# Kernel tuning notes

Hardware: AMD Instinct MI355X
Metric: run time of the kernel (lower is better)

## Reference

```python
import jax, jax.numpy as jnp
import numpy as np

B, N, E = 64, 512, 8192          # graphs, nodes per graph, edges per graph
F_IN, H, C = 128, 128, 10        # in features, hidden, classes
K1, K2 = 256, 128                # dense pool cluster counts: ceil(.5*N), ceil(.5*K1)
EPS = 1e-15


def setup_inputs():
    key = jax.random.key(0)
    keys = jax.random.split(key, 32)
    it = iter(keys)
    def w(shape, fan_in):
        return jax.random.normal(next(it), shape, jnp.float32) / np.sqrt(fan_in)
    x = jax.random.normal(next(it), (B * N, F_IN), jnp.float32)
    src_l = jax.random.randint(next(it), (B, E), 0, N)
    dst_l = jax.random.randint(next(it), (B, E), 0, N)
    off = (jnp.arange(B) * N)[:, None]
    src = (src_l + off).reshape(-1).astype(jnp.int32)
    dst = (dst_l + off).reshape(-1).astype(jnp.int32)
    return dict(
        x=x, src=src, dst=dst,
        conv0_wr=w((F_IN, H), F_IN), conv0_wroot=w((F_IN, H), F_IN), conv0_b=jnp.zeros((H,), jnp.float32),
        sconv2_wr=w((H, H), H), sconv2_wroot=w((H, H), H), sconv2_b=jnp.zeros((H,), jnp.float32),
        sconv3_wr=w((H, H), H), sconv3_wroot=w((H, H), H), sconv3_b=jnp.zeros((H,), jnp.float32),
        sage1_wr=w((H, H), H), sage1_wroot=w((H, H), H), sage1_b=jnp.zeros((H,), jnp.float32),
        sage2_wr=w((H, H), H), sage2_wroot=w((H, H), H), sage2_b=jnp.zeros((H,), jnp.float32),
        pool0_w=w((H, K1), H), pool0_b=jnp.zeros((K1,), jnp.float32),
        pool1_w=w((H, K2), H), pool1_b=jnp.zeros((K2,), jnp.float32),
        p1=w((H,), H), p2=w((H,), H), p3=w((H,), H),
        lin1_1_w=w((2 * H, H), 2 * H), lin1_1_b=jnp.zeros((H,), jnp.float32),
        lin1_w=w((H, H), H), lin1_b=jnp.zeros((H,), jnp.float32),
        lin2_w=w((2 * H, C), 2 * H), lin2_b=jnp.zeros((C,), jnp.float32),
    )


def _graph_conv(x, src, dst, emask, wr, wroot, b, n):
    # PyG GraphConv: lin_rel(sum_j x_j) + lin_root(x_i); invalid edges masked to 0.
    msg = x[src] * emask[:, None]
    agg = jax.ops.segment_sum(msg, dst, num_segments=n)
    return agg @ wr + x @ wroot + b


def _topk_pool(x, score_w, src, dst, emask, n_per_graph, k):
    # TopK pooling (MPoolS): score = x.w/||w||, keep top ratio*n per graph, gate by tanh(score).
    score = x @ score_w / (jnp.linalg.norm(score_w) + 1e-16)
    idx = jax.lax.top_k(score.reshape(B, n_per_graph), k)[1]
    perm = (idx + (jnp.arange(B) * n_per_graph)[:, None]).reshape(-1)
    new_x = x[perm] * jnp.tanh(score[perm])[:, None]
    new_id = jnp.full((B * n_per_graph,), -1, jnp.int32).at[perm].set(
        jnp.arange(B * k, dtype=jnp.int32))
    ns, nd = new_id[src], new_id[dst]
    valid = (ns >= 0) & (nd >= 0) & (emask > 0)
    return new_x, jnp.where(valid, ns, 0), jnp.where(valid, nd, 0), valid.astype(x.dtype)


def _readout(x, k):
    # gmp || gap per graph (nodes are contiguous, k per graph)
    xr = x.reshape(B, k, -1)
    return jnp.concatenate([xr.max(axis=1), xr.mean(axis=1)], axis=-1)


def _dense_sage(x, adj, wr, wroot, b):
    agg = (adj @ x) / jnp.clip(adj.sum(-1, keepdims=True), 1.0, None)
    return agg @ wr + x @ wroot + b


def _dense_mincut_pool(x, adj, s):
    s = jax.nn.softmax(s, axis=-1)
    k = s.shape[-1]
    out = jnp.einsum('bnk,bnf->bkf', s, x)
    out_adj = jnp.einsum('bnk,bnm,bml->bkl', s, adj, s)
    mincut_num = jnp.trace(out_adj, axis1=-2, axis2=-1)
    deg = adj.sum(-1)
    mincut_den = jnp.einsum('bn,bnk,bnk->b', deg, s, s)
    mc = -jnp.mean(mincut_num / (mincut_den + EPS))
    ss = jnp.einsum('bnk,bnl->bkl', s, s)
    ss_n = jnp.linalg.norm(ss, axis=(1, 2), keepdims=True)
    eye = jnp.eye(k, dtype=x.dtype)
    o = jnp.mean(jnp.linalg.norm(ss / (ss_n + EPS) - eye / jnp.sqrt(k), axis=(1, 2)))
    di = jnp.arange(k)
    out_adj = out_adj.at[:, di, di].set(0.0)
    dpool = jnp.sqrt(out_adj.sum(-1)) + EPS
    out_adj = out_adj / dpool[:, :, None] / dpool[:, None, :]
    return out, out_adj, mc, o


def _forward(x, src, dst, conv0_wr, conv0_wroot, conv0_b, sconv2_wr, sconv2_wroot, sconv2_b,
             sconv3_wr, sconv3_wroot, sconv3_b, sage1_wr, sage1_wroot, sage1_b,
             sage2_wr, sage2_wroot, sage2_b, pool0_w, pool0_b, pool1_w, pool1_b,
             p1, p2, p3, lin1_1_w, lin1_1_b, lin1_w, lin1_b, lin2_w, lin2_b):
    relu = jax.nn.relu
    e0 = jnp.ones((src.shape[0],), x.dtype)
    x0 = relu(_graph_conv(x, src, dst, e0, conv0_wr, conv0_wroot, conv0_b, B * N))
    # ---- sparse (MPoolS / top-k) branch, stage 1 ----
    sx, s1, d1, m1 = _topk_pool(x0, p1, src, dst, e0, N, N // 2)
    sx1 = _readout(sx, N // 2)
    # ---- dense (DiffPool-style) branch ----
    xd = x0.reshape(B, N, H)                               # to_dense_batch (full mask)
    g = src // N
    adj = jnp.zeros((B, N, N), x.dtype).at[g, src % N, dst % N].add(1.0)  # to_dense_adj
    s = xd @ pool0_w + pool0_b
    xd, adj, mc, o = _dense_mincut_pool(xd, adj, s)
    xd = relu(_dense_sage(xd, adj, sage1_wr, sage1_wroot, sage1_b))
    s = xd @ pool1_w + pool1_b
    xd, adj, mc2, o2 = _dense_mincut_pool(xd, adj, s)
    mc, o = mc + mc2, o + o2
    xd = _dense_sage(xd, adj, sage2_wr, sage2_wroot, sage2_b)
    xg = relu(xd.mean(axis=1) @ lin1_w + lin1_b)
    # ---- sparse branch, stages 2 and 3 ----
    sx = relu(_graph_conv(sx, s1, d1, m1, sconv2_wr, sconv2_wroot, sconv2_b, B * (N // 2)))
    sx, s2, d2, m2 = _topk_pool(sx, p2, s1, d1, m1, N // 2, N // 4)
    sx2 = _readout(sx, N // 4)
    sx = relu(_graph_conv(sx, s2, d2, m2, sconv3_wr, sconv3_wroot, sconv3_b, B * (N // 4)))
    sx, s3, d3, m3 = _topk_pool(sx, p3, s2, d2, m2, N // 4, N // 8)
    sx3 = _readout(sx, N // 8)
    sxr = relu((sx1 + sx2 + sx3) @ lin1_1_w + lin1_1_b)
    logits = jnp.concatenate([sxr, xg], axis=-1) @ lin2_w + lin2_b
    return logits, mc, o


def reference(x, src, dst, conv0_wr, conv0_wroot, conv0_b, sconv2_wr, sconv2_wroot, sconv2_b,
              sconv3_wr, sconv3_wroot, sconv3_b, sage1_wr, sage1_wroot, sage1_b,
              sage2_wr, sage2_wroot, sage2_b, pool0_w, pool0_b, pool1_w, pool1_b,
              p1, p2, p3, lin1_1_w, lin1_1_b, lin1_w, lin1_b, lin2_w, lin2_b):
    return _forward(x, src, dst, conv0_wr, conv0_wroot, conv0_b, sconv2_wr, sconv2_wroot,
                    sconv2_b, sconv3_wr, sconv3_wroot, sconv3_b, sage1_wr, sage1_wroot,
                    sage1_b, sage2_wr, sage2_wroot, sage2_b, pool0_w, pool0_b, pool1_w,
                    pool1_b, p1, p2, p3, lin1_1_w, lin1_1_b, lin1_w, lin1_b, lin2_w, lin2_b)
```

## Files before the change

### kernel.cpp

```cpp
#include <hip/hip_runtime.h>
#include <math.h>

#define NGRAPH 64
#define NE 524288
#define EPG 8192
#define TSZ 2560

typedef short s16x8 __attribute__((ext_vector_type(8)));
typedef float f32x4 __attribute__((ext_vector_type(4)));

__device__ inline unsigned short f2bf(float f) {
    unsigned int u = __float_as_uint(f);
    return (unsigned short)((u + 0x7FFFu + ((u >> 16) & 1u)) >> 16);
}
__device__ inline float bf2f(unsigned short h) {
    return __uint_as_float((unsigned int)h << 16);
}
__device__ inline unsigned int f2pk(float v) {
    unsigned short h = f2bf(v);
    return (unsigned int)h | ((unsigned int)f2bf(v - bf2f(h)) << 16);
}

__global__ void edge_count2(const int* __restrict__ keyA, int* __restrict__ cntA,
                            const int* __restrict__ keyB, int* __restrict__ cntB) {
    int e = blockIdx.x * 256 + threadIdx.x;
    if (e >= NE) return;
    if (blockIdx.y == 0) atomicAdd(&cntA[keyA[e]], 1);
    else                 atomicAdd(&cntB[keyB[e]], 1);
}

__device__ inline void scan_body(const int* __restrict__ counts, int* __restrict__ offs,
                                 int* __restrict__ cursor, int nPerGraph,
                                 float* __restrict__ degOut, int* s) {
    const int g = blockIdx.x, t = threadIdx.x;
    int v = (t < nPerGraph) ? counts[g * nPerGraph + t] : 0;
    s[t] = v; __syncthreads();
    for (int d = 1; d < 512; d <<= 1) {
        int u = (t >= d) ? s[t - d] : 0;
        __syncthreads();
        s[t] += u;
        __syncthreads();
    }
    if (t < nPerGraph) {
        int o = g * EPG + s[t] - v;
        offs[g * nPerGraph + t] = o;
        cursor[g * nPerGraph + t] = o;
        if (degOut) degOut[g * nPerGraph + t] = (float)v;
    }
}

__global__ __launch_bounds__(512) void scan_offsets(const int* __restrict__ counts,
        int* __restrict__ offs, int* __restrict__ cursor, int nPerGraph,
        float* __restrict__ degOut) {
    __shared__ int s[512];
    scan_body(counts, offs, cursor, nPerGraph, degOut, s);
}

__global__ __launch_bounds__(512) void scan_offsets2(
        const int* __restrict__ cA, int* __restrict__ oA, int* __restrict__ uA,
        const int* __restrict__ cB, int* __restrict__ oB, int* __restrict__ uB,
        int nPerGraph, float* __restrict__ degB) {
    __shared__ int s[512];
    if (blockIdx.y == 0) scan_body(cA, oA, uA, nPerGraph, nullptr, s);
    else                 scan_body(cB, oB, uB, nPerGraph, degB, s);
}

__global__ void edge_fill(const int* __restrict__ key, const int* __restrict__ payload,
                          const float* __restrict__ mask, int* __restrict__ cursor,
                          int* __restrict__ elist) {
    int e = blockIdx.x * 256 + threadIdx.x;
    if (e < NE && (!mask || mask[e] > 0.f)) {
        int p = atomicAdd(&cursor[key[e]], 1);
        elist[p] = payload[e];
    }
}

__global__ void edge_fill2(const int* __restrict__ kA, const int* __restrict__ pA,
                           int* __restrict__ uA, int* __restrict__ eA,
                           const int* __restrict__ kB, const int* __restrict__ pB,
                           int* __restrict__ uB, int* __restrict__ eB) {
    int e = blockIdx.x * 256 + threadIdx.x;
    if (e >= NE) return;
    if (blockIdx.y == 0) { int p = atomicAdd(&uA[kA[e]], 1); eA[p] = pA[e]; }
    else                 { int p = atomicAdd(&uB[kB[e]], 1); eB[p] = pB[e]; }
}

__device__ inline void addpk(float4& acc, uint4 u) {
    acc.x += __uint_as_float(u.x << 16) + __uint_as_float(u.x & 0xffff0000u);
    acc.y += __uint_as_float(u.y << 16) + __uint_as_float(u.y & 0xffff0000u);
    acc.z += __uint_as_float(u.z << 16) + __uint_as_float(u.z & 0xffff0000u);
    acc.w += __uint_as_float(u.w << 16) + __uint_as_float(u.w & 0xffff0000u);
}

__global__ __launch_bounds__(256) void gather_csr(
    const float* __restrict__ xf, const unsigned int* __restrict__ xp, int Fx,
    const int* __restrict__ offs, const int* __restrict__ cnts,
    const int* __restrict__ elist,
    unsigned int* __restrict__ opk,
    int totRows, int rowsPerGraph)
{
    const int gid = (blockIdx.x * 256 + threadIdx.x) >> 5;
    const int lane = threadIdx.x & 31;
    const int csh = (Fx == 256) ? 1 : 0;
    const int rid = gid >> csh;
    const int c0 = (gid & ((1 << csh) - 1)) << 7;
    if (rid >= totRows) return;
    const int row = (rid & 63) * rowsPerGraph + (rid >> 6);
    const int beg = offs[row];
    const int n = cnts[row];
    const long long co = (long long)c0 + (lane << 2);
    float4 acc = make_float4(0.f, 0.f, 0.f, 0.f);
    int j = 0;
    if (xp) {
        for (; j + 4 <= n; j += 4) {
            const int n0 = elist[beg + j], n1 = elist[beg + j + 1];
            const int n2 = elist[beg + j + 2], n3 = elist[beg + j + 3];
            const uint4 u0 = *(const uint4*)&xp[(long long)n0 * Fx + co];
            const uint4 u1 = *(const uint4*)&xp[(long long)n1 * Fx + co];
            const uint4 u2 = *(const uint4*)&xp[(long long)n2 * Fx + co];
            const uint4 u3 = *(const uint4*)&xp[(long long)n3 * Fx + co];
            addpk(acc, u0); addpk(acc, u1); addpk(acc, u2); addpk(acc, u3);
        }
        for (; j < n; ++j)
            addpk(acc, *(const uint4*)&xp[(long long)elist[beg + j] * Fx + co]);
    } else {
        for (; j + 4 <= n; j += 4) {
            const int n0 = elist[beg + j], n1 = elist[beg + j + 1];
            const int n2 = elist[beg + j + 2], n3 = elist[beg + j + 3];
            const float4 v0 = *(const float4*)&xf[(long long)n0 * Fx + co];
            const float4 v1 = *(const float4*)&xf[(long long)n1 * Fx + co];
            const float4 v2 = *(const float4*)&xf[(long long)n2 * Fx + co];
            const float4 v3 = *(const float4*)&xf[(long long)n3 * Fx + co];
            acc.x += v0.x + v1.x + v2.x + v3.x;
            acc.y += v0.y + v1.y + v2.y + v3.y;
            acc.z += v0.z + v1.z + v2.z + v3.z;
            acc.w += v0.w + v1.w + v2.w + v3.w;
        }
        for (; j < n; ++j) {
            const float4 v = *(const float4*)&xf[(long long)elist[beg + j] * Fx + co];
            acc.x += v.x; acc.y += v.y; acc.z += v.z; acc.w += v.w;
        }
    }
    uint4 pk;
    pk.x = f2pk(acc.x); pk.y = f2pk(acc.y); pk.z = f2pk(acc.z); pk.w = f2pk(acc.w);
    *(uint4*)&opk[(long long)row * Fx + co] = pk;
}

struct WSpec {
    const float* w1; const float* w2; int K1; int K2; int Nn;
    unsigned short* oh; unsigned short* ol;
};

__global__ void wconv_all(WSpec s0, WSpec s1, WSpec s2, WSpec s3, WSpec s4, WSpec s5, WSpec s6) {
    WSpec s;
    switch (blockIdx.y) {
        case 0: s = s0; break; case 1: s = s1; break; case 2: s = s2; break;
        case 3: s = s3; break; case 4: s = s4; break; case 5: s = s5; break;
        default: s = s6; break;
    }
    int idx = blockIdx.x * 256 + threadIdx.x;
    int Kt = s.K1 + s.K2;
    if (idx >= s.Nn * Kt) return;
    int n = idx / Kt, k = idx - n * Kt;
    float v = (k < s.K1) ? s.w1[(long long)k * s.Nn + n] : s.w2[(long long)(k - s.K1) * s.Nn + n];
    unsigned short h = f2bf(v);
    s.oh[idx] = h;
    s.ol[idx] = f2bf(v - __uint_as_float((unsigned int)h << 16));
}

__device__ inline void stageN_split(const float* __restrict__ src, int ldk, int k0,
                                    short* lds, int tid) {
    const int r = tid >> 2, kq = (tid & 3) << 3;
    const float* p = src + (long long)r * ldk + k0 + kq;
    float v[8];
    *(float4*)v = *(const float4*)p;
    *(float4*)(v + 4) = *(const float4*)(p + 4);
    s16x8 hv, lv;
    #pragma unroll
    for (int i = 0; i < 8; ++i) {
        unsigned short h = f2bf(v[i]);
        float hf = __uint_as_float((unsigned int)h << 16);
        hv[i] = (short)h;
        lv[i] = (short)f2bf(v[i] - hf);
    }
    *(s16x8*)(lds + r * 40 + kq) = hv;
    *(s16x8*)(lds + TSZ + r * 40 + kq) = lv;
}

__device__ inline void stageN_pk(const unsigned int* __restrict__ src, int ldk, int k0,
                                 short* lds, int tid) {
    const int r = tid >> 2, kq = (tid & 3) << 3;
    const unsigned int* p = src + (long long)r * ldk + k0 + kq;
    uint4 a = *(const uint4*)p;
    uint4 b = *(const uint4*)(p + 4);
    uint4 hw, lw;
    hw.x = (a.x & 0xffffu) | (a.y << 16);
    hw.y = (a.z & 0xffffu) | (a.w << 16);
    hw.z = (b.x & 0xffffu) | (b.y << 16);
    hw.w = (b.z & 0xffffu) | (b.w << 16);
    lw.x = (a.x >> 16) | (a.y & 0xffff0000u);
    lw.y = (a.z >> 16) | (a.w & 0xffff0000u);
    lw.z = (b.x >> 16) | (b.y & 0xffff0000u);
    lw.w = (b.z >> 16) | (b.w & 0xffff0000u);
    *(uint4*)(lds + r * 40 + kq) = hw;
    *(uint4*)(lds + TSZ + r * 40 + kq) = lw;
}

__device__ inline void stageT_pk(const unsigned int* __restrict__ P,
                                 int ldm, int k0, int m0, short* lds, int tid) {
    const int kp = tid >> 4, mc = tid & 15;
    const int k = kp << 1;
    const unsigned int* p0 = P + (long long)(k0 + k) * ldm + m0 + mc;
    const unsigned int* p1 = p0 + ldm;
    #pragma unroll
    for (int i = 0; i < 4; ++i) {
        unsigned int e0 = p0[i << 4], e1 = p1[i << 4];
        const int o = (mc + (i << 4)) * 40 + k;
        *(unsigned int*)(lds + o) = (e0 & 0xffffu) | (e1 << 16);
        *(unsigned int*)(lds + o + TSZ) = (e0 >> 16) | (e1 & 0xffff0000u);
    }
}

__device__ inline void stageW_split(const unsigned short* __restrict__ wh,
                                    const unsigned short* __restrict__ wl, int ldk,
                                    int n0, int k0, short* lds, int tid) {
    const int r = tid >> 2, kq = (tid & 3) << 3;
    *(s16x8*)(lds + r * 40 + kq) = *(const s16x8*)(wh + (long long)(n0 + r) * ldk + k0 + kq);
    *(s16x8*)(lds + TSZ + r * 40 + kq) = *(const s16x8*)(wl + (long long)(n0 + r) * ldk + k0 + kq);
}

__device__ inline void loadT8(const unsigned int* __restrict__ P, int ldm, int k0, int m0,
                              int tid, unsigned int (&r)[8]) {
    const int kp = tid >> 4, mc = tid & 15;
    const int k = kp << 1;
    const unsigned int* p0 = P + (long long)(k0 + k) * ldm + m0 + mc;
    const unsigned int* p1 = p0 + ldm;
    #pragma unroll
    for (int i = 0; i < 4; ++i) { r[i] = p0[i << 4]; r[4 + i] = p1[i << 4]; }
}
__device__ inline void storeT8(short* lds, int tid, const unsigned int (&r)[8]) {
    const int kp = tid >> 4, mc = tid & 15;
    const int k = kp << 1;
    #pragma unroll
    for (int i = 0; i < 4; ++i) {
        unsigned int e0 = r[i], e1 = r[4 + i];
        const int o = (mc + (i << 4)) * 40 + k;
        *(unsigned int*)(lds + o) = (e0 & 0xffffu) | (e1 << 16);
        *(unsigned int*)(lds + o + TSZ) = (e0 >> 16) | (e1 & 0xffff0000u);
    }
}
__device__ inline void storeT8_hi(short* lds, int tid, const unsigned int (&r)[8]) {
    const int kp = tid >> 4, mc = tid & 15;
    const int k = kp << 1;
    #pragma unroll
    for (int i = 0; i < 4; ++i)
        *(unsigned int*)(lds + (mc + (i << 4)) * 40 + k) =
            (r[i] & 0xffffu) | (r[4 + i] << 16);
}

__device__ inline void mfma_split(const short* As, const short* Bs, int wm, int wn,
                                  int l15, int quad, f32x4 (&acc)[2][2]) {
    const int ko = quad << 3;
    s16x8 ah[2], al[2], bh[2], bl[2];
    #pragma unroll
    for (int i = 0; i < 2; ++i) {
        const int ra = (wm + (i << 4) + l15) * 40 + ko;
        const int rb = (wn + (i << 4) + l15) * 40 + ko;
        ah[i] = *(const s16x8*)&As[ra];
        al[i] = *(const s16x8*)&As[TSZ + ra];
        bh[i] = *(const s16x8*)&Bs[rb];
        bl[i] = *(const s16x8*)&Bs[TSZ + rb];
    }
    #pragma unroll
    for (int mi = 0; mi < 2; ++mi)
    #pragma unroll
    for (int ni = 0; ni < 2; ++ni) {
        f32x4 c = acc[mi][ni];
        c = __builtin_amdgcn_mfma_f32_16x16x32_bf16(ah[mi], bh[ni], c, 0, 0, 0);
        c = __builtin_amdgcn_mfma_f32_16x16x32_bf16(ah[mi], bl[ni], c, 0, 0, 0);
        c = __builtin_amdgcn_mfma_f32_16x16x32_bf16(al[mi], bh[ni], c, 0, 0, 0);
        acc[mi][ni] = c;
    }
}

__device__ inline void mfma_hi(const short* As, const short* Bs, int wm, int wn,
                               int l15, int quad, f32x4 (&acc)[2][2]) {
    const int ko = quad << 3;
    s16x8 ah[2], bh[2];
    #pragma unroll
    for (int i = 0; i < 2; ++i) {
        ah[i] = *(const s16x8*)&As[(wm + (i << 4) + l15) * 40 + ko];
        bh[i] = *(const s16x8*)&Bs[(wn + (i << 4) + l15) * 40 + ko];
    }
    #pragma unroll
    for (int mi = 0; mi < 2; ++mi)
    #pragma unroll
    for (int ni = 0; ni < 2; ++ni)
        acc[mi][ni] = __builtin_amdgcn_mfma_f32_16x16x32_bf16(ah[mi], bh[ni], acc[mi][ni], 0, 0, 0);
}

__global__ __launch_bounds__(256) void gemm_aw(
    const unsigned int* __restrict__ A1p, const float* __restrict__ A1f, int K1,
    const unsigned int* __restrict__ A2p, const float* __restrict__ A2f, int K2,
    const unsigned short* __restrict__ Wh, const unsigned short* __restrict__ Wl,
    const float* __restrict__ bias, float* __restrict__ C,
    unsigned int* __restrict__ Cpk,
    int Nn, int doRelu)
{
    __shared__ short As[2 * TSZ], Bs[2 * TSZ];
    const int m0 = blockIdx.y << 6, n0 = blockIdx.x << 6;
    const int tid = threadIdx.x, lane = tid & 63, wv = tid >> 6;
    const int l15 = lane & 15, quad = lane >> 4;
    const int wm = (wv & 1) << 5, wn = (wv >> 1) << 5;
    f32x4 acc[2][2] = {};
    const int Kt = K1 + K2;
    for (int k0 = 0; k0 < Kt; k0 += 32) {
        if (k0 < K1) {
            if (A1p) stageN_pk(A1p + (long long)m0 * K1, K1, k0, As, tid);
            else     stageN_split(A1f + (long long)m0 * K1, K1, k0, As, tid);
        } else {
            if (A2p) stageN_pk(A2p + (long long)m0 * K2, K2, k0 - K1, As, tid);
            else     stageN_split(A2f + (long long)m0 * K2, K2, k0 - K1, As, tid);
        }
        stageW_split(Wh, Wl, Kt, n0, k0, Bs, tid);
        __syncthreads();
        mfma_split(As, Bs, wm, wn, l15, quad, acc);
        __syncthreads();
    }
    #pragma unroll
    for (int mi = 0; mi < 2; ++mi)
    #pragma unroll
    for (int ni = 0; ni < 2; ++ni) {
        const int col = n0 + wn + (ni << 4) + l15;
        const float bv = bias ? bias[col] : 0.f;
        #pragma unroll
        for (int r = 0; r < 4; ++r) {
            const int row = m0 + wm + (mi << 4) + (quad << 2) + r;
            float v = acc[mi][ni][r] + bv;
            if (doRelu) v = fmaxf(v, 0.f);
            if (C)   C[(long long)row * Nn + col] = v;
            if (Cpk) Cpk[(long long)row * Nn + col] = f2pk(v);
        }
    }
}

struct TTSet {
    const unsigned int* Bp;
    float* C; unsigned int* Cpk; float* fro;
    int Nn; int dual;
    long long sB, sC;
};

__global__ __launch_bounds__(256) void gemm_tt(
    const unsigned int* __restrict__ Ap, int Kd, int Mm, long long sA,
    int zsplit, TTSet t0, TTSet t1)
{
    __shared__ short As[2 * TSZ], Bs[2 * TSZ], A2s[TSZ];
    __shared__ float redf[4];
    const int z = blockIdx.x;
    int nz = blockIdx.z;
    const TTSet tt = (nz < zsplit) ? t0 : t1;
    if (blockIdx.z >= zsplit) nz -= zsplit;
    const unsigned int* Apz = Ap + (long long)z * sA;
    const unsigned int* Bpz = tt.Bp + (long long)z * tt.sB;
    const int m0 = blockIdx.y << 6, n0 = nz << 6;
    const int tid = threadIdx.x, lane = tid & 63, wv = tid >> 6;
    const int l15 = lane & 15, quad = lane >> 4;
    const int wm = (wv & 1) << 5, wn = (wv >> 1) << 5;
    const int fw = tt.dual ? ((m0 < n0) ? 2 : ((m0 == n0) ? 1 : 0)) : 0;
    f32x4 acc[2][2] = {};
    f32x4 accA[2][2] = {};
    unsigned int ra[8], rb[8], rh[8];
    loadT8(Apz, Mm, 0, m0, tid, ra);
    loadT8(Bpz, tt.Nn, 0, n0, tid, rb);
    if (fw) loadT8(Apz, Mm, 0, n0, tid, rh);
    for (int k0 = 0; k0 < Kd; k0 += 32) {
        storeT8(As, tid, ra);
        storeT8(Bs, tid, rb);
        if (fw) storeT8_hi(A2s, tid, rh);
        __syncthreads();
        const int kn = k0 + 32;
        if (kn < Kd) {
            loadT8(Apz, Mm, kn, m0, tid, ra);
            loadT8(Bpz, tt.Nn, kn, n0, tid, rb);
            if (fw) loadT8(Apz, Mm, kn, n0, tid, rh);
        }
        mfma_split(As, Bs, wm, wn, l15, quad, acc);
        if (fw) mfma_hi(As, A2s, wm, wn, l15, quad, accA);
        __syncthreads();
    }
    float* Cp = tt.C ? tt.C + (long long)z * tt.sC : nullptr;
    unsigned int* Ckp = tt.Cpk ? tt.Cpk + (long long)z * tt.sC : nullptr;
    #pragma unroll
    for (int mi = 0; mi < 2; ++mi)
    #pragma unroll
    for (int ni = 0; ni < 2; ++ni) {
        const int col = n0 + wn + (ni << 4) + l15;
        #pragma unroll
        for (int r = 0; r < 4; ++r) {
            const int row = m0 + wm + (mi << 4) + (quad << 2) + r;
            const float v = acc[mi][ni][r];
            if (Cp)  Cp[(long long)row * tt.Nn + col] = v;
            if (Ckp) Ckp[(long long)row * tt.Nn + col] = f2pk(v);
        }
    }
    if (fw) {
        float s = 0.f;
        #pragma unroll
        for (int mi = 0; mi < 2; ++mi)
        #pragma unroll
        for (int ni = 0; ni < 2; ++ni)
        #pragma unroll
        for (int r = 0; r < 4; ++r) s += accA[mi][ni][r] * accA[mi][ni][r];
        s *= (float)fw;
        for (int off = 32; off; off >>= 1) s += __shfl_xor(s, off);
        if (lane == 0) redf[wv] = s;
        __syncthreads();
        if (tid == 0) atomicAdd(&tt.fro[z], redf[0] + redf[1] + redf[2] + redf[3]);
    }
}

__global__ __launch_bounds__(256) void gemm_nt(
    const unsigned short* __restrict__ Ah, const unsigned short* __restrict__ Al,
    const unsigned int* __restrict__ Bp,
    float* __restrict__ C, unsigned int* __restrict__ Cpk,
    const float* __restrict__ rscale, int rsn,
    int Kd, int Nn, long long sA, long long sB, long long sC)
{
    __shared__ short As[2 * TSZ], Bs[2 * TSZ];
    const int z = blockIdx.x;
    const int m0 = blockIdx.y << 6, n0 = blockIdx.z << 6;
    const unsigned short* Aph = Ah + (long long)z * sA;
    const unsigned short* Apl = Al + (long long)z * sA;
    const unsigned int* Bpz = Bp + (long long)z * sB;
    const int tid = threadIdx.x, lane = tid & 63, wv = tid >> 6;
    const int l15 = lane & 15, quad = lane >> 4;
    const int wm = (wv & 1) << 5, wn = (wv >> 1) << 5;
    f32x4 acc[2][2] = {};
    for (int k0 = 0; k0 < Kd; k0 += 32) {
        stageW_split(Aph, Apl, Kd, m0, k0, As, tid);
        stageT_pk(Bpz, Nn, k0, n0, Bs, tid);
        __syncthreads();
        mfma_split(As, Bs, wm, wn, l15, quad, acc);
        __syncthreads();
    }
    #pragma unroll
    for (int mi = 0; mi < 2; ++mi)
    #pragma unroll
    for (int ni = 0; ni < 2; ++ni) {
        const int col = n0 + wn + (ni << 4) + l15;
        #pragma unroll
        for (int r = 0; r < 4; ++r) {
            const int row = m0 + wm + (mi << 4) + (quad << 2) + r;
            float v = acc[mi][ni][r];
            if (rscale) v *= rscale[z * rsn + row];
            if (C)   C[(long long)z * sC + (long long)row * Nn + col] = v;
            if (Cpk) Cpk[(long long)z * sC + (long long)row * Nn + col] = f2pk(v);
        }
    }
}

__global__ __launch_bounds__(256) void softmax_rows_wave(
    const float* __restrict__ sm, int L,
    const float* __restrict__ deg,
    float* __restrict__ rowq2, float* __restrict__ rowdq2, int totRows,
    unsigned int* __restrict__ opk)
{
    const int wid = (blockIdx.x * 256 + threadIdx.x) >> 6;
    const int lane = threadIdx.x & 63;
    if (wid >= totRows) return;
    const float* rowp = sm + (long long)wid * L;
    const int nv = L >> 6;
    float v[4];
    if (nv == 4) {
        float4 t = *(const float4*)&rowp[lane << 2];
        v[0] = t.x; v[1] = t.y; v[2] = t.z; v[3] = t.w;
    } else {
        float2 t = *(const float2*)&rowp[lane << 1];
        v[0] = t.x; v[1] = t.y;
    }
    float mx = v[0];
    for (int i = 1; i < nv; ++i) mx = fmaxf(mx, v[i]);
    for (int off = 32; off; off >>= 1) mx = fmaxf(mx, __shfl_xor(mx, off));
    float s = 0.f;
    for (int i = 0; i < nv; ++i) { v[i] = expf(v[i] - mx); s += v[i]; }
    for (int off = 32; off; off >>= 1) s += __shfl_xor(s, off);
    const float inv = 1.f / s;
    float q2 = 0.f;
    for (int i = 0; i < nv; ++i) { float p = v[i] * inv; v[i] = p; q2 += p * p; }
    const long long rb = (long long)wid * L;
    if (nv == 4) {
        uint4 pk;
        pk.x = f2pk(v[0]); pk.y = f2pk(v[1]); pk.z = f2pk(v[2]); pk.w = f2pk(v[3]);
        *(uint4*)&opk[rb + (lane << 2)] = pk;
    } else {
        uint2 pk;
        pk.x = f2pk(v[0]); pk.y = f2pk(v[1]);
        *(uint2*)&opk[rb + (lane << 1)] = pk;
    }
    for (int off = 32; off; off >>= 1) q2 += __shfl_xor(q2, off);
    if (lane == 0) { rowq2[wid] = q2; rowdq2[wid] = deg[wid] * q2; }
}

__global__ __launch_bounds__(256) void reduce2_pergraph(
    const float* __restrict__ a, const float* __restrict__ b, int rowsPerGraph,
    float* __restrict__ outA, float* __restrict__ outB)
{
    __shared__ float redA[4], redB[4];
    const int g = blockIdx.x, t = threadIdx.x;
    float sa = 0.f, sb = 0.f;
    for (int i = t; i < rowsPerGraph; i += 256) {
        sa += a[g * rowsPerGraph + i];
        if (b) sb += b[g * rowsPerGraph + i];
    }
    for (int off = 32; off; off >>= 1) { sa += __shfl_xor(sa, off); sb += __shfl_xor(sb, off); }
    const int wv = t >> 6;
    if ((t & 63) == 0) { redA[wv] = sa; redB[wv] = sb; }
    __syncthreads();
    if (t == 0) {
        outA[g] = redA[0] + redA[1] + redA[2] + redA[3];
        if (outB) outB[g] = redB[0] + redB[1] + redB[2] + redB[3];
    }
}

__global__ __launch_bounds__(1024) void adjnorm(
    const float* __restrict__ adj, int K,
    float* __restrict__ trace_out,
    float* __restrict__ rowsum, float* __restrict__ rscale,
    unsigned short* __restrict__ oh, unsigned short* __restrict__ ol)
{
    __shared__ float dpoolL[256];
    __shared__ float trL;
    const int g = blockIdx.x, tid = threadIdx.x;
    const int wv = tid >> 6, lane = tid & 63;
    if (tid == 0) trL = 0.f;
    __syncthreads();
    const int rowsPerWave = K >> 4;
    const int nv = K >> 6;
    float trpart = 0.f;
    for (int rr = 0; rr < rowsPerWave; ++rr) {
        const int r = wv * rowsPerWave + rr;
        const float* rowp = adj + (long long)(g * K + r) * K;
        float s = 0.f, dval = 0.f;
        for (int q = 0; q < nv; ++q) {
            int c = lane + (q << 6);
            float v = rowp[c];
            if (c == r) { dval = v; v = 0.f; }
            s += v;
        }
        for (int off = 32; off; off >>= 1) s += __shfl_xor(s, off);
        for (int off = 32; off; off >>= 1) dval += __shfl_xor(dval, off);
        if (lane == 0) { dpoolL[r] = sqrtf(s) + 1e-15f; trpart += dval; }
    }
    if (lane == 0) atomicAdd(&trL, trpart);
    __syncthreads();
    if (tid == 0) trace_out[g] = trL;
    for (int rr = 0; rr < rowsPerWave; ++rr) {
        const int r = wv * rowsPerWave + rr;
        const int wid = g * K + r;
        const float* rowp = adj + (long long)wid * K;
        const float inv_r = 1.f / dpoolL[r];
        float s = 0.f;
        for (int q = 0; q < nv; ++q) {
            int c = lane + (q << 6);
            float a = rowp[c];
            if (c == r) a = 0.f;
            float v = a * inv_r / dpoolL[c];
            s += v;
            unsigned short h = f2bf(v);
            oh[(long long)wid * K + c] = h;
            ol[(long long)wid * K + c] = f2bf(v - bf2f(h));
        }
        for (int off = 32; off; off >>= 1) s += __shfl_xor(s, off);
        if (lane == 0) { rowsum[wid] = s; rscale[wid] = 1.f / fmaxf(s, 1.f); }
    }
}

__global__ __launch_bounds__(512) void topk_fused(
    const float* __restrict__ x, const float* __restrict__ p, int n, int k,
    int* __restrict__ new_id, float* __restrict__ outx,
    float* __restrict__ sxsum, int* __restrict__ cntZero)
{
    __shared__ float sc[512];
    __shared__ int pref[512];
    __shared__ int   selL[256];
    __shared__ float gateL[256];
    __shared__ float red[1024];
    const int g = blockIdx.x, tid = threadIdx.x;
    if (cntZero && tid < k) cntZero[g * k + tid] = 0;
    float myScore = 0.f;
    if (tid < n) {
        const float* xr = x + (long long)(g * n + tid) * 128;
        float pn2 = 0.f, d = 0.f;
        #pragma unroll 4
        for (int f = 0; f < 128; f += 4) {
            float4 pv = *(const float4*)&p[f];
            float4 v = *(const float4*)&xr[f];
            pn2 += pv.x * pv.x + pv.y * pv.y + pv.z * pv.z + pv.w * pv.w;
            d += v.x * pv.x + v.y * pv.y + v.z * pv.z + v.w * pv.w;
        }
        myScore = d / (sqrtf(pn2) + 1e-16f);
        sc[tid] = myScore;
    }
    __syncthreads();
    int keep = 0;
    if (tid < n) {
        const float si = myScore;
        int rank = 0;
        for (int j = 0; j < n; j += 4) {
            float4 s4 = *(const float4*)&sc[j];
            rank += (s4.x > si) || (s4.x == si && (j + 0) < tid);
            rank += (s4.y > si) || (s4.y == si && (j + 1) < tid);
            rank += (s4.z > si) || (s4.z == si && (j + 2) < tid);
            rank += (s4.w > si) || (s4.w == si && (j + 3) < tid);
        }
        keep = rank < k;
    }
    pref[tid] = keep;
    __syncthreads();
    for (int d = 1; d < 512; d <<= 1) {
        int u = (tid >= d) ? pref[tid - d] : 0;
        __syncthreads();
        pref[tid] += u;
        __syncthreads();
    }
    if (tid < n) {
        if (keep) {
            int pos = pref[tid] - 1;
            new_id[g * n + tid] = g * k + pos;
            selL[pos] = g * n + tid;
            gateL[pos] = tanhf(myScore);
        } else new_id[g * n + tid] = -1;
    }
    __syncthreads();
    const int f = tid & 127, grp = tid >> 7;
    float mx = -INFINITY, sm = 0.f;
    for (int r = grp; r < k; r += 4) {
        float v = x[(long long)selL[r] * 128 + f] * gateL[r];
        outx[(long long)(g * k + r) * 128 + f] = v;
        mx = fmaxf(mx, v); sm += v;
    }
    red[grp * 128 + f] = mx;
    red[512 + grp * 128 + f] = sm;
    __syncthreads();
    if (tid < 128) {
        float m = fmaxf(fmaxf(red[f], red[128 + f]), fmaxf(red[256 + f], red[384 + f]));
        float s2 = red[512 + f] + red[640 + f] + red[768 + f] + red[896 + f];
        sxsum[g * 256 + f] += m;
        sxsum[g * 256 + 128 + f] += s2 / k;
    }
}

__global__ void remap_edges_count(const int* __restrict__ s, const int* __restrict__ d,
                                  const float* __restrict__ m, const int* __restrict__ new_id,
                                  int* __restrict__ so, int* __restrict__ do_,
                                  float* __restrict__ mo, int* __restrict__ counts) {
    int e = blockIdx.x * blockDim.x + threadIdx.x;
    if (e >= NE) return;
    int ns = new_id[s[e]], nd = new_id[d[e]];
    bool v = (ns >= 0) && (nd >= 0) && (m ? (m[e] > 0.f) : true);
    so[e] = v ? ns : 0; do_[e] = v ? nd : 0; mo[e] = v ? 1.f : 0.f;
    if (v) atomicAdd(&counts[nd], 1);
}

__global__ void final_head(const float* __restrict__ sxsum, const float* __restrict__ w11,
                           const float* __restrict__ b11,
                           const float* __restrict__ xd2, const float* __restrict__ l1w,
                           const float* __restrict__ l1b,
                           const float* __restrict__ w2, const float* __restrict__ b2,
                           const float* __restrict__ accs, float* __restrict__ out) {
    __shared__ float meanv[128];
    __shared__ float sin_[256];
    __shared__ float cat[256];
    __shared__ float rm[2], ro[2];
    int b = blockIdx.x, t = threadIdx.x;
    {
        float s = 0.f;
        for (int n = 0; n < 128; n++) s += xd2[(long long)(b * 128 + n) * 128 + t];
        meanv[t] = s / 128.f;
    }
    if (b == 0) {
        int wvi = t >> 6, lane = t & 63;
        const float* acc = accs + wvi * 256;
        float sqrtk = wvi ? sqrtf(128.f) : 16.f;
        float numv = acc[lane], denv = acc[64 + lane], trv = acc[128 + lane], frov = acc[192 + lane];
        float mcb = numv / (denv + 1e-15f);
        float ssn = sqrtf(frov) + 1e-15f;
        float ob = sqrtf(fmaxf(frov / (ssn * ssn) - 2.f * trv / (ssn * sqrtk) + 1.f, 0.f));
        for (int off = 32; off; off >>= 1) { mcb += __shfl_down(mcb, off); ob += __shfl_down(ob, off); }
        if (lane == 0) { rm[wvi] = mcb; ro[wvi] = ob; }
        __syncthreads();
        if (t == 0) {
            out[640] = -(rm[0] + rm[1]) / 64.f;
            out[641] = (ro[0] + ro[1]) / 64.f;
        }
    }
    sin_[t] = sxsum[b * 256 + t];
    sin_[t + 128] = sxsum[b * 256 + 128 + t];
    __syncthreads();
    float acc = b11[t];
    for (int i = 0; i < 256; i++) acc += sin_[i] * w11[i * 128 + t];
    cat[t] = fmaxf(acc, 0.f);
    float xga = l1b[t];
    for (int i = 0; i < 128; i++) xga += meanv[i] * l1w[i * 128 + t];
    cat[128 + t] = fmaxf(xga, 0.f);
    __syncthreads();
    if (t < 10) {
        float a = b2[t];
        for (int i = 0; i < 256; i++) a += cat[i] * w2[i * 10 + t];
        out[b * 10 + t] = a;
    }
}

extern "C" void kernel_launch(void* const* d_in, const int* in_sizes, int n_in,
                              void* d_out, int out_size, void* d_ws, size_t ws_size,
                              hipStream_t stream) {
    const float* x         = (const float*)d_in[0];
    const int*   src       = (const int*)d_in[1];
    const int*   dst       = (const int*)d_in[2];
    const float* conv0_wr  = (const float*)d_in[3];
    const float* conv0_wrt = (const float*)d_in[4];
    const float* conv0_b   = (const float*)d_in[5];
    const float* sc2_wr    = (const float*)d_in[6];
    const float* sc2_wrt   = (const float*)d_in[7];
    const float* sc2_b     = (const float*)d_in[8];
    const float* sc3_wr    = (const float*)d_in[9];
    const float* sc3_wrt   = (const float*)d_in[10];
    const float* sc3_b     = (const float*)d_in[11];
    const float* sg1_wr    = (const float*)d_in[12];
    const float* sg1_wrt   = (const float*)d_in[13];
    const float* sg1_b     = (const float*)d_in[14];
    const float* sg2_wr    = (const float*)d_in[15];
    const float* sg2_wrt   = (const float*)d_in[16];
    const float* sg2_b     = (const float*)d_in[17];
    const float* pool0_w   = (const float*)d_in[18];
    const float* pool0_b   = (const float*)d_in[19];
    const float* pool1_w   = (const float*)d_in[20];
    const float* pool1_b   = (const float*)d_in[21];
    const float* p1        = (const float*)d_in[22];
    const float* p2        = (const float*)d_in[23];
    const float* p3        = (const float*)d_in[24];
    const float* l11_w     = (const float*)d_in[25];
    const float* l11_b     = (const float*)d_in[26];
    const float* l1_w      = (const float*)d_in[27];
    const float* l1_b      = (const float*)d_in[28];
    const float* l2_w      = (const float*)d_in[29];
    const float* l2_b      = (const float*)d_in[30];
    float* out = (float*)d_out;

    char* w = (char*)d_ws;
    const unsigned long long MBy = 1ull << 20;
    float* x0    = (float*)(w + 0);
    float* BIG1  = (float*)(w + 16 * MBy);
    float* BIG2  = (float*)(w + 48 * MBy);
    float* agg   = (float*)(w + 80 * MBy);
    float* adj1  = (float*)(w + 104 * MBy);
    int*   s1    = (int*)(w + 120 * MBy);
    int*   d1    = (int*)(w + 122 * MBy);
    float* m1    = (float*)(w + 124 * MBy);
    int*   s2e   = (int*)(w + 126 * MBy);
    int*   d2e   = (int*)(w + 128 * MBy);
    float* m2e   = (float*)(w + 130 * MBy);
    char*  misc  = w + 132 * MBy;
    float* rowq2  = (float*)(misc);
    float* rowdq2 = (float*)(misc + 128 * 1024);
    int*   newid = (int*)(misc + 256 * 1024);
    float* deg   = (float*)(misc + 384 * 1024);
    float* rowsum2 = (float*)(misc + 576 * 1024);
    float* rscale2 = (float*)(misc + 640 * 1024);
    float* rowsum3 = (float*)(misc + 736 * 1024);
    float* rscale3 = (float*)(misc + 768 * 1024);
    float* accs    = (float*)(misc + 800 * 1024);
    float* sxsum   = (float*)(misc + 900 * 1024);

    unsigned short* wt_sg1h   = (unsigned short*)(misc + 1024 * 1024);
    unsigned short* wt_sg1l   = wt_sg1h + 32768;
    unsigned short* wt_sg2h   = wt_sg1l + 32768;
    unsigned short* wt_sg2l   = wt_sg2h + 32768;
    unsigned short* wt_pool0h = wt_sg2l + 32768;
    unsigned short* wt_pool0l = wt_pool0h + 32768;
    unsigned short* wt_pool1h = wt_pool0l + 32768;
    unsigned short* wt_pool1l = wt_pool1h + 32768;
    unsigned short* wt_c0h    = wt_pool1l + 32768;
    unsigned short* wt_c0l    = wt_c0h + 32768;
    unsigned short* wt_sc2h   = wt_c0l + 32768;
    unsigned short* wt_sc2l   = wt_sc2h + 32768;
    unsigned short* wt_sc3h   = wt_sc2l + 32768;
    unsigned short* wt_sc3l   = wt_sc3h + 32768;

    float* s_sm  = BIG1;
    unsigned int* Tbp = (unsigned int*)BIG2;
    float* s2sm  = BIG2 + 4 * 1024 * 1024;
    unsigned int* T2p = (unsigned int*)((char*)BIG2 + 24 * MBy);
    float* adj2b = BIG1 + 1024 * 1024;
    float* xd2   = BIG1 + 2 * 1024 * 1024;
    float* sxA   = BIG1 + 3 * 1024 * 1024;
    float* sxE   = BIG1 + 5 * 1024 * 1024;
    float* sxB   = x0;
    float* sxC   = x0 + 2 * 1024 * 1024;
    float* sxD   = x0 + 3 * 1024 * 1024;

    unsigned int* s_smp = (unsigned int*)(w + 136 * MBy);
    unsigned int* x0p   = (unsigned int*)(w + 168 * MBy);
    unsigned int* ox1p  = (unsigned int*)(w + 184 * MBy);
    unsigned int* xd1p  = (unsigned int*)(w + 192 * MBy);
    unsigned int* s2p   = (unsigned int*)(w + 200 * MBy);
    unsigned int* ox2p  = (unsigned int*)(w + 208 * MBy);
    unsigned short* a1h = (unsigned short*)(w + 212 * MBy);
    unsigned short* a1l = (unsigned short*)(w + 220 * MBy);
    unsigned short* a2h = (unsigned short*)(w + 228 * MBy);
    unsigned short* a2l = (unsigned short*)(w + 230 * MBy);
    unsigned int* AXp   = (unsigned int*)(w + 232 * MBy);
    unsigned int* AXp2  = (unsigned int*)(w + 240 * MBy);

    unsigned int* aggp  = (unsigned int*)agg;
    unsigned int* agg2p = (unsigned int*)agg;
    unsigned int* agg3p = (unsigned int*)agg;

    char* adjc = (char*)adj1;
    int* elA  = (int*)(adjc + 0);
    int* elB  = (int*)(adjc + 2 * MBy);
    int* cntA = (int*)(adjc + 4 * MBy);
    int* cntB = (int*)(adjc + 4 * MBy + 128 * 1024);
    int* offA = (int*)(adjc + 4 * MBy + 256 * 1024);
    int* curA = (int*)(adjc + 4 * MBy + 384 * 1024);
    int* offB = (int*)(adjc + 4 * MBy + 512 * 1024);
    int* curB = (int*)(adjc + 4 * MBy + 640 * 1024);
    char* aggc = (char*)agg;
    int* elC  = (int*)(aggc + 8 * MBy);
    int* elD  = (int*)(aggc + 10 * MBy);
    int* cntC = (int*)(aggc + 12 * MBy);
    int* offC = (int*)(aggc + 12 * MBy + 256 * 1024);
    int* curC = (int*)(aggc + 12 * MBy + 512 * 1024);
    int* cntD = (int*)(aggc + 13 * MBy);
    int* offD = (int*)(aggc + 13 * MBy + 256 * 1024);
    int* curD = (int*)(aggc + 13 * MBy + 512 * 1024);

    hipMemsetAsync(accs, 0, 520 * sizeof(float), stream);
    hipMemsetAsync(sxsum, 0, 16384 * sizeof(float), stream);
    hipMemsetAsync(cntA, 0, 65536 * sizeof(int), stream);

    {
        WSpec a{sg1_wr, sg1_wrt, 128, 128, 128, wt_sg1h, wt_sg1l};
        WSpec b{sg2_wr, sg2_wrt, 128, 128, 128, wt_sg2h, wt_sg2l};
        WSpec c{pool0_w, nullptr, 128, 0, 256, wt_pool0h, wt_pool0l};
        WSpec d{pool1_w, nullptr, 128, 0, 128, wt_pool1h, wt_pool1l};
        WSpec e{conv0_wr, conv0_wrt, 128, 128, 128, wt_c0h, wt_c0l};
        WSpec f{sc2_wr, sc2_wrt, 128, 128, 128, wt_sc2h, wt_sc2l};
        WSpec g{sc3_wr, sc3_wrt, 128, 128, 128, wt_sc3h, wt_sc3l};
        wconv_all<<<dim3(128, 7), 256, 0, stream>>>(a, b, c, d, e, f, g);
    }

    edge_count2<<<dim3(2048, 2), 256, 0, stream>>>(dst, cntA, src, cntB);
    scan_offsets2<<<dim3(64, 2), 512, 0, stream>>>(cntA, offA, curA, cntB, offB, curB, 512, deg);
    edge_fill2<<<dim3(2048, 2), 256, 0, stream>>>(dst, src, curA, elA, src, dst, curB, elB);

    gather_csr<<<4096, 256, 0, stream>>>(x, nullptr, 128, offA, cntA, elA, aggp, 32768, 512);
    gemm_aw<<<dim3(2, 512), 256, 0, stream>>>(aggp, nullptr, 128, nullptr, x, 128,
        wt_c0h, wt_c0l, conv0_b, x0, x0p, 128, 1);

    gemm_aw<<<dim3(4, 512), 256, 0, stream>>>(x0p, nullptr, 128, nullptr, nullptr, 0,
        wt_pool0h, wt_pool0l, pool0_b, s_sm, nullptr, 256, 0);
    softmax_rows_wave<<<8192, 256, 0, stream>>>(s_sm, 256, deg, rowq2, rowdq2, 32768, s_smp);
    reduce2_pergraph<<<64, 256, 0, stream>>>(rowq2, rowdq2, 512, accs + 128, accs + 64);
    gather_csr<<<8192, 256, 0, stream>>>(nullptr, s_smp, 256, offB, cntB, elB, Tbp, 32768, 512);
    {
        TTSet t0{x0p, nullptr, ox1p, nullptr, 128, 0, 512 * 128, 256 * 128};
        TTSet t1{Tbp, adj1, nullptr, accs + 192, 256, 1, 512 * 256, 256 * 256};
        gemm_tt<<<dim3(64, 4, 6), 256, 0, stream>>>(s_smp, 512, 256, 512 * 256, 2, t0, t1);
    }
    adjnorm<<<64, 1024, 0, stream>>>(adj1, 256, accs + 0, rowsum2, rscale2, a1h, a1l);
    gemm_nt<<<dim3(64, 4, 2), 256, 0, stream>>>(a1h, a1l, ox1p, nullptr, AXp, rscale2, 256,
        256, 128, 256 * 256, 256 * 128, 256 * 128);
    gemm_aw<<<dim3(2, 256), 256, 0, stream>>>(AXp, nullptr, 128, ox1p, nullptr, 128,
        wt_sg1h, wt_sg1l, sg1_b, nullptr, xd1p, 128, 1);
    gemm_aw<<<dim3(2, 256), 256, 0, stream>>>(xd1p, nullptr, 128, nullptr, nullptr, 0,
        wt_pool1h, wt_pool1l, pool1_b, s2sm, nullptr, 128, 0);
    softmax_rows_wave<<<4096, 256, 0, stream>>>(s2sm, 128, rowsum2, rowq2, rowdq2, 16384, s2p);
    reduce2_pergraph<<<64, 256, 0, stream>>>(rowq2, rowdq2, 256, accs + 384, accs + 320);
    gemm_nt<<<dim3(64, 4, 2), 256, 0, stream>>>(a1h, a1l, s2p, nullptr, T2p, nullptr, 0,
        256, 128, 256 * 256, 256 * 128, 256 * 128);
    {
        TTSet t0{xd1p, nullptr, ox2p, nullptr, 128, 0, 256 * 128, 128 * 128};
        TTSet t1{T2p, adj2b, nullptr, accs + 448, 128, 1, 256 * 128, 128 * 128};
        gemm_tt<<<dim3(64, 2, 4), 256, 0, stream>>>(s2p, 256, 128, 256 * 128, 2, t0, t1);
    }
    adjnorm<<<64, 1024, 0, stream>>>(adj2b, 128, accs + 256, rowsum3, rscale3, a2h, a2l);
    gemm_nt<<<dim3(64, 2, 2), 256, 0, stream>>>(a2h, a2l, ox2p, nullptr, AXp2, rscale3, 128,
        128, 128, 128 * 128, 128 * 128, 128 * 128);
    gemm_aw<<<dim3(2, 128), 256, 0, stream>>>(AXp2, nullptr, 128, ox2p, nullptr, 128,
        wt_sg2h, wt_sg2l, sg2_b, xd2, nullptr, 128, 0);

    topk_fused<<<64, 512, 0, stream>>>(x0, p1, 512, 256, newid, sxA, sxsum, cntC);
    remap_edges_count<<<2048, 256, 0, stream>>>(src, dst, nullptr, newid, s1, d1, m1, cntC);
    scan_offsets<<<64, 512, 0, stream>>>(cntC, offC, curC, 256, nullptr);
    edge_fill<<<2048, 256, 0, stream>>>(d1, s1, m1, curC, elC);
    gather_csr<<<2048, 256, 0, stream>>>(sxA, nullptr, 128, offC, cntC, elC, agg2p, 16384, 256);
    gemm_aw<<<dim3(2, 256), 256, 0, stream>>>(agg2p, nullptr, 128, nullptr, sxA, 128,
        wt_sc2h, wt_sc2l, sc2_b, sxB, nullptr, 128, 1);
    topk_fused<<<64, 512, 0, stream>>>(sxB, p2, 256, 128, newid, sxC, sxsum, cntD);
    remap_edges_count<<<2048, 256, 0, stream>>>(s1, d1, m1, newid, s2e, d2e, m2e, cntD);
    scan_offsets<<<64, 512, 0, stream>>>(cntD, offD, curD, 128, nullptr);
    edge_fill<<<2048, 256, 0, stream>>>(d2e, s2e, m2e, curD, elD);
    gather_csr<<<1024, 256, 0, stream>>>(sxC, nullptr, 128, offD, cntD, elD, agg3p, 8192, 128);
    gemm_aw<<<dim3(2, 128), 256, 0, stream>>>(agg3p, nullptr, 128, nullptr, sxC, 128,
        wt_sc3h, wt_sc3l, sc3_b, sxD, nullptr, 128, 1);
    topk_fused<<<64, 512, 0, stream>>>(sxD, p3, 128, 64, newid, sxE, sxsum, nullptr);

    final_head<<<64, 128, 0, stream>>>(sxsum, l11_w, l11_b, xd2, l1_w, l1_b,
        l2_w, l2_b, accs, out);
}
```

Baseline: 645.5 us.

## Fuse adjacency row sums and diagonal into gemm_tt epilogue; prefetch B in gemm_nt

The gemm_tt epilogue now computes per-row sums of the pooled adjacency through wave shuffles and atomics, and records the diagonal entries. adjnorm uses these instead of making a first full pass over the adjacency matrix, which removes one read of adj. gemm_nt also register-prefetches the next B tile while the current tile is in MFMA, overlapping global loads with compute. The cost is extra atomics, two memsets, and the fact that floating-point atomics make the row sums order-dependent.

```diff
diff --git a/kernel.cpp b/kernel.cpp
--- a/kernel.cpp
+++ b/kernel.cpp
@@ -349,6 +349,7 @@
     float* C; unsigned int* Cpk; float* fro;
     int Nn; int dual;
     long long sB, sC;
+    float* rsum; float* rdiag;
 };
 
 __global__ __launch_bounds__(256) void gemm_tt(
@@ -404,6 +405,35 @@
             if (Ckp) Ckp[(long long)row * tt.Nn + col] = f2pk(v);
         }
     }
+    if (tt.rsum) {
+        #pragma unroll
+        for (int mi = 0; mi < 2; ++mi) {
+            #pragma unroll
+            for (int r = 0; r < 4; ++r) {
+                float rs = acc[mi][0][r] + acc[mi][1][r];
+                rs += __shfl_xor(rs, 1);
+                rs += __shfl_xor(rs, 2);
+                rs += __shfl_xor(rs, 4);
+                rs += __shfl_xor(rs, 8);
+                if (l15 == 0) {
+                    const int row = m0 + wm + (mi << 4) + (quad << 2) + r;
+                    atomicAdd(&tt.rsum[z * tt.Nn + row], rs);
+                }
+            }
+        }
+        if (tt.rdiag && m0 == n0) {
+            #pragma unroll
+            for (int mi = 0; mi < 2; ++mi)
+            #pragma unroll
+            for (int ni = 0; ni < 2; ++ni)
+            #pragma unroll
+            for (int r = 0; r < 4; ++r) {
+                const int rr = wm + (mi << 4) + (quad << 2) + r;
+                const int cc = wn + (ni << 4) + l15;
+                if (rr == cc) tt.rdiag[z * tt.Nn + m0 + rr] = acc[mi][ni][r];
+            }
+        }
+    }
     if (fw) {
         float s = 0.f;
         #pragma unroll
@@ -437,10 +467,14 @@
     const int l15 = lane & 15, quad = lane >> 4;
     const int wm = (wv & 1) << 5, wn = (wv >> 1) << 5;
     f32x4 acc[2][2] = {};
+    unsigned int rb[8];
+    loadT8(Bpz, Nn, 0, n0, tid, rb);
     for (int k0 = 0; k0 < Kd; k0 += 32) {
         stageW_split(Aph, Apl, Kd, m0, k0, As, tid);
-        stageT_pk(Bpz, Nn, k0, n0, Bs, tid);
-        __syncthreads();
+        storeT8(Bs, tid, rb);
+        __syncthreads();
+        const int kn = k0 + 32;
+        if (kn < Kd) loadT8(Bpz, Nn, kn, n0, tid, rb);
         mfma_split(As, Bs, wm, wn, l15, quad, acc);
         __syncthreads();
     }
@@ -525,36 +559,32 @@
 
 __global__ __launch_bounds__(1024) void adjnorm(
     const float* __restrict__ adj, int K,
+    const float* __restrict__ rsumIn, const float* __restrict__ rdiagIn,
     float* __restrict__ trace_out,
     float* __restrict__ rowsum, float* __restrict__ rscale,
     unsigned short* __restrict__ oh, unsigned short* __restrict__ ol)
 {
     __shared__ float dpoolL[256];
-    __shared__ float trL;
+    __shared__ float redt[16];
     const int g = blockIdx.x, tid = threadIdx.x;
     const int wv = tid >> 6, lane = tid & 63;
-    if (tid == 0) trL = 0.f;
+    float trp = 0.f;
+    for (int r = tid; r < K; r += 1024) {
+        float dv = rdiagIn[g * K + r];
+        dpoolL[r] = sqrtf(rsumIn[g * K + r] - dv) + 1e-15f;
+        trp += dv;
+    }
+    for (int off = 32; off; off >>= 1) trp += __shfl_xor(trp, off);
+    if (lane == 0) redt[wv] = trp;
     __syncthreads();
+    if (tid == 0) {
+        float t = 0.f;
+        #pragma unroll
+        for (int i = 0; i < 16; ++i) t += redt[i];
+        trace_out[g] = t;
+    }
     const int rowsPerWave = K >> 4;
     const int nv = K >> 6;
-    float trpart = 0.f;
-    for (int rr = 0; rr < rowsPerWave; ++rr) {
-        const int r = wv * rowsPerWave + rr;
-        const float* rowp = adj + (long long)(g * K + r) * K;
-        float s = 0.f, dval = 0.f;
-        for (int q = 0; q < nv; ++q) {
-            int c = lane + (q << 6);
-            float v = rowp[c];
-            if (c == r) { dval = v; v = 0.f; }
-            s += v;
-        }
-        for (int off = 32; off; off >>= 1) s += __shfl_xor(s, off);
-        for (int off = 32; off; off >>= 1) dval += __shfl_xor(dval, off);
-        if (lane == 0) { dpoolL[r] = sqrtf(s) + 1e-15f; trpart += dval; }
-    }
-    if (lane == 0) atomicAdd(&trL, trpart);
-    __syncthreads();
-    if (tid == 0) trace_out[g] = trL;
     for (int rr = 0; rr < rowsPerWave; ++rr) {
         const int r = wv * rowsPerWave + rr;
         const int wid = g * K + r;
@@ -788,6 +818,11 @@
     unsigned short* wt_sc3h   = wt_sc2l + 32768;
     unsigned short* wt_sc3l   = wt_sc3h + 32768;
 
+    float* rsum1  = (float*)(misc + 2048 * 1024);
+    float* rdiag1 = (float*)(misc + 2112 * 1024);
+    float* rsum2  = (float*)(misc + 2176 * 1024);
+    float* rdiag2 = (float*)(misc + 2208 * 1024);
+
     float* s_sm  = BIG1;
     unsigned int* Tbp = (unsigned int*)BIG2;
     float* s2sm  = BIG2 + 4 * 1024 * 1024;
@@ -839,6 +874,8 @@
     hipMemsetAsync(accs, 0, 520 * sizeof(float), stream);
     hipMemsetAsync(sxsum, 0, 16384 * sizeof(float), stream);
     hipMemsetAsync(cntA, 0, 65536 * sizeof(int), stream);
+    hipMemsetAsync(rsum1, 0, 128 * 1024, stream);
+    hipMemsetAsync(rsum2, 0, 64 * 1024, stream);
 
     {
         WSpec a{sg1_wr, sg1_wrt, 128, 128, 128, wt_sg1h, wt_sg1l};
@@ -865,11 +902,12 @@
     reduce2_pergraph<<<64, 256, 0, stream>>>(rowq2, rowdq2, 512, accs + 128, accs + 64);
     gather_csr<<<8192, 256, 0, stream>>>(nullptr, s_smp, 256, offB, cntB, elB, Tbp, 32768, 512);
     {
-        TTSet t0{x0p, nullptr, ox1p, nullptr, 128, 0, 512 * 128, 256 * 128};
-        TTSet t1{Tbp, adj1, nullptr, accs + 192, 256, 1, 512 * 256, 256 * 256};
+        TTSet t0{x0p, nullptr, ox1p, nullptr, 128, 0, 512 * 128, 256 * 128, nullptr, nullptr};
+        TTSet t1{Tbp, adj1, nullptr, accs + 192, 256, 1, 512 * 256, 256 * 256, rsum1, rdiag1};
         gemm_tt<<<dim3(64, 4, 6), 256, 0, stream>>>(s_smp, 512, 256, 512 * 256, 2, t0, t1);
     }
-    adjnorm<<<64, 1024, 0, stream>>>(adj1, 256, accs + 0, rowsum2, rscale2, a1h, a1l);
+    adjnorm<<<64, 1024, 0, stream>>>(adj1, 256, rsum1, rdiag1, accs + 0,
+        rowsum2, rscale2, a1h, a1l);
     gemm_nt<<<dim3(64, 4, 2), 256, 0, stream>>>(a1h, a1l, ox1p, nullptr, AXp, rscale2, 256,
         256, 128, 256 * 256, 256 * 128, 256 * 128);
     gemm_aw<<<dim3(2, 256), 256, 0, stream>>>(AXp, nullptr, 128, ox1p, nullptr, 128,
@@ -881,11 +919,12 @@
     gemm_nt<<<dim3(64, 4, 2), 256, 0, stream>>>(a1h, a1l, s2p, nullptr, T2p, nullptr, 0,
         256, 128, 256 * 256, 256 * 128, 256 * 128);
     {
-        TTSet t0{xd1p, nullptr, ox2p, nullptr, 128, 0, 256 * 128, 128 * 128};
-        TTSet t1{T2p, adj2b, nullptr, accs + 448, 128, 1, 256 * 128, 128 * 128};
+        TTSet t0{xd1p, nullptr, ox2p, nullptr, 128, 0, 256 * 128, 128 * 128, nullptr, nullptr};
+        TTSet t1{T2p, adj2b, nullptr, accs + 448, 128, 1, 256 * 128, 128 * 128, rsum2, rdiag2};
         gemm_tt<<<dim3(64, 2, 4), 256, 0, stream>>>(s2p, 256, 128, 256 * 128, 2, t0, t1);
     }
-    adjnorm<<<64, 1024, 0, stream>>>(adj2b, 128, accs + 256, rowsum3, rscale3, a2h, a2l);
+    adjnorm<<<64, 1024, 0, stream>>>(adj2b, 128, rsum2, rdiag2, accs + 256,
+        rowsum3, rscale3, a2h, a2l);
     gemm_nt<<<dim3(64, 2, 2), 256, 0, stream>>>(a2h, a2l, ox2p, nullptr, AXp2, rscale3, 128,
         128, 128, 128 * 128, 128 * 128, 128 * 128);
     gemm_aw<<<dim3(2, 128), 256, 0, stream>>>(AXp2, nullptr, 128, ox2p, nullptr, 128,
```

Measured after the change: 629.2 us. 1.03x faster.
